# Performance work log

Measured on AMD Instinct MI355X. Metric: run time of the kernel, lower is better.

The kernel has to match this reference:

```python
import jax, jax.numpy as jnp
import numpy as np

B, S, D, H = 2, 2048, 2048, 16
HD = D // H  # head_dim = 128
ROPE_BASE = 10000.0


def _rope_tables(seq_len, head_dim, base, dtype):
    inv_freq = 1.0 / (base ** (jnp.arange(0, head_dim, 2, dtype=jnp.float32) / head_dim))
    t = jnp.arange(seq_len, dtype=jnp.float32)
    freqs = jnp.einsum('s,d->sd', t, inv_freq)           # [S, HD/2]
    emb = jnp.concatenate([freqs, freqs], axis=-1)        # [S, HD]
    return jnp.cos(emb).astype(dtype), jnp.sin(emb).astype(dtype)


def _rotate_half(x):
    half = x.shape[-1] // 2
    return jnp.concatenate([-x[..., half:], x[..., :half]], axis=-1)


def setup_inputs() -> dict:
    key = jax.random.key(0)
    kx, kq, kk, kv, ko = jax.random.split(key, 5)
    std = 0.02
    return {
        'x': jax.random.normal(kx, (B, S, D), dtype=jnp.float32),
        'Wq': jax.random.normal(kq, (D, D), dtype=jnp.float32) * std,
        'Wk': jax.random.normal(kk, (D, D), dtype=jnp.float32) * std,
        'Wv': jax.random.normal(kv, (D, D), dtype=jnp.float32) * std,
        'Wo': jax.random.normal(ko, (D, D), dtype=jnp.float32) * std,
    }


def reference(x, Wq, Wk, Wv, Wo):
    b, s, d = x.shape
    scale = HD ** -0.5
    # projections (nn.Linear: x @ W.T), split heads -> [b, h, s, hd]
    q = (x @ Wq.T).reshape(b, s, H, HD).transpose(0, 2, 1, 3)
    k = (x @ Wk.T).reshape(b, s, H, HD).transpose(0, 2, 1, 3)
    v = (x @ Wv.T).reshape(b, s, H, HD).transpose(0, 2, 1, 3)
    cos, sin = _rope_tables(s, HD, ROPE_BASE, x.dtype)    # [s, hd]
    q = q * cos + _rotate_half(q) * sin
    k = k * cos + _rotate_half(k) * sin
    scores = jnp.einsum('bhqd,bhkd->bhqk', q, k) * scale  # [b,h,s,s]
    causal = jnp.triu(jnp.ones((s, s), dtype=bool), k=1)
    scores = jnp.where(causal, jnp.float32(-jnp.inf).astype(scores.dtype), scores)
    attn = jax.nn.softmax(scores, axis=-1)
    out = jnp.einsum('bhqk,bhkd->bhqd', attn, v)
    out = out.transpose(0, 2, 1, 3).reshape(b, s, d)
    return out @ Wo.T
```

## Files before the change

### kernel.cpp

```cpp
#include <hip/hip_runtime.h>
#include <hip/hip_bf16.h>
#include <cstdint>
#include <cstddef>

#define B_ 2
#define S_ 2048
#define D_ 2048
#define H_ 16
#define HD_ 128

typedef __bf16 bf16_t;
typedef __bf16 bf16x8 __attribute__((ext_vector_type(8)));
typedef __bf16 bf16x4 __attribute__((ext_vector_type(4)));
typedef short s16x4 __attribute__((ext_vector_type(4)));
typedef float f32x4 __attribute__((ext_vector_type(4)));

__device__ __forceinline__ void async16(const bf16_t* g, bf16_t* l) {
    __builtin_amdgcn_global_load_lds(
        (const __attribute__((address_space(1))) unsigned int*)g,
        (__attribute__((address_space(3))) unsigned int*)l, 16, 0, 0);
}

__device__ __forceinline__ f32x4 mfma16x16x16_bf16(bf16x4 a, bf16x4 b, f32x4 c) {
#if __has_builtin(__builtin_amdgcn_mfma_f32_16x16x16_bf16)
    return __builtin_amdgcn_mfma_f32_16x16x16_bf16(a, b, c, 0, 0, 0);
#elif __has_builtin(__builtin_amdgcn_mfma_f32_16x16x16bf16_1k)
    return __builtin_amdgcn_mfma_f32_16x16x16bf16_1k(
        __builtin_bit_cast(s16x4, a), __builtin_bit_cast(s16x4, b), c, 0, 0, 0);
#else
    f32x4 d = c;
    asm("v_mfma_f32_16x16x16_bf16 %0, %1, %2, %0" : "+v"(d) : "v"(a), "v"(b));
    return d;
#endif
}

__global__ void f2b_multi(const float* __restrict__ x, const float* __restrict__ wq,
                          const float* __restrict__ wk, const float* __restrict__ wv,
                          const float* __restrict__ wo, bf16_t* __restrict__ xb,
                          bf16_t* __restrict__ wqb, bf16_t* __restrict__ wkb,
                          bf16_t* __restrict__ wvb, bf16_t* __restrict__ wob) {
    const float* in; bf16_t* out;
    float sc = 1.0f;
    switch (blockIdx.y) {
        case 0: in = x;            out = xb;            break;
        case 1: in = x + 4194304;  out = xb + 4194304;  break;
        case 2: in = wq;           out = wqb; sc = 0.08838834764831845f; break;
        case 3: in = wk;           out = wkb;           break;
        case 4: in = wv;           out = wvb;           break;
        default: in = wo;          out = wob;           break;
    }
    int i = (blockIdx.x * blockDim.x + threadIdx.x) * 4;
    float4 v = *(const float4*)(in + i);
    bf16x4 o = { (bf16_t)(v.x * sc), (bf16_t)(v.y * sc), (bf16_t)(v.z * sc), (bf16_t)(v.w * sc) };
    *(bf16x4*)(out + i) = o;
}

__global__ void rope_kernel(bf16_t* __restrict__ q, bf16_t* __restrict__ k) {
    int idx = blockIdx.x * blockDim.x + threadIdx.x;
    bf16_t* p = (blockIdx.y == 0) ? q : k;
    int i0 = (idx & 7) * 8;
    int rest = idx >> 3;
    int h = rest & (H_ - 1);
    int row = rest >> 4;
    int s = row & (S_ - 1);
    size_t base = (size_t)row * D_ + (size_t)h * HD_ + i0;
    bf16x8 x0 = *(bf16x8*)(p + base);
    bf16x8 x1 = *(bf16x8*)(p + base + 64);
    bf16x8 o0, o1;
#pragma unroll
    for (int j = 0; j < 8; ++j) {
        float inv = __expf(-(float)(i0 + j) * 0.14391156831212787f);
        float ang = (float)s * inv;
        float sn, c;
        __sincosf(ang, &sn, &c);
        float a = (float)x0[j], bb = (float)x1[j];
        o0[j] = (bf16_t)(a * c - bb * sn);
        o1[j] = (bf16_t)(bb * c + a * sn);
    }
    *(bf16x8*)(p + base) = o0;
    *(bf16x8*)(p + base + 64) = o1;
}


__global__ __launch_bounds__(256) void gemm_qkv(const bf16_t* __restrict__ A,
                                                const bf16_t* __restrict__ Wq,
                                                const bf16_t* __restrict__ Wk,
                                                const bf16_t* __restrict__ Wv,
                                                bf16_t* __restrict__ qb,
                                                bf16_t* __restrict__ kb,
                                                bf16_t* __restrict__ vtb) {
    __shared__ __align__(16) bf16_t As[128 * 64];
    __shared__ __align__(16) bf16_t Bs[128 * 64];
    const int K = D_;
    int t = threadIdx.x;
    int w = t >> 6, lane = t & 63, lo = lane & 15, hi = lane >> 4;
    int seg = blockIdx.x >> 4;
    int n0 = (blockIdx.x & 15) * 128;
    int m0 = blockIdx.y * 128;
    const bf16_t* Bt = (seg == 0) ? Wq : (seg == 1) ? Wk : Wv;
    int wm = (w & 1) * 64, wn = (w >> 1) * 64;
    f32x4 acc[4][4] = {};
    int srow = w * 32 + (lane >> 3);
    int scol = ((lane & 7) ^ (lane >> 3)) * 8;
    const bf16_t* gA = A  + (size_t)(m0 + srow) * K + scol;
    const bf16_t* gB = Bt + (size_t)(n0 + srow) * K + scol;
    bf16_t* lA = As + w * 2048 + lane * 8;
    bf16_t* lB = Bs + w * 2048 + lane * 8;
    for (int k0 = 0; k0 < K; k0 += 64) {
#pragma unroll
        for (int i = 0; i < 4; ++i) {
            async16(gA + (size_t)(i * 8) * K + k0, lA + i * 512);
            async16(gB + (size_t)(i * 8) * K + k0, lB + i * 512);
        }
        __syncthreads();
#pragma unroll
        for (int kk = 0; kk < 2; ++kk) {
            bf16x8 af[4], bfr[4];
            int pc = (kk * 4 + hi) ^ (lo & 7);
#pragma unroll
            for (int ms = 0; ms < 4; ++ms)
                af[ms] = *(const bf16x8*)(As + (wm + ms * 16 + lo) * 64 + pc * 8);
#pragma unroll
            for (int ns = 0; ns < 4; ++ns)
                bfr[ns] = *(const bf16x8*)(Bs + (wn + ns * 16 + lo) * 64 + pc * 8);
#pragma unroll
            for (int ms = 0; ms < 4; ++ms)
#pragma unroll
                for (int ns = 0; ns < 4; ++ns)
                    acc[ms][ns] = __builtin_amdgcn_mfma_f32_16x16x32_bf16(af[ms], bfr[ns], acc[ms][ns], 0, 0, 0);
        }
        __syncthreads();
    }
    if (seg < 2) {
        bf16_t* C = (seg == 0) ? qb : kb;
#pragma unroll
        for (int ms = 0; ms < 4; ++ms)
#pragma unroll
            for (int ns = 0; ns < 4; ++ns)
#pragma unroll
                for (int r = 0; r < 4; ++r)
                    C[(size_t)(m0 + wm + ms * 16 + hi * 4 + r) * D_ + n0 + wn + ns * 16 + lo] = (bf16_t)acc[ms][ns][r];
    } else {
#pragma unroll
        for (int ms = 0; ms < 4; ++ms) {
            int mrow = m0 + wm + ms * 16 + hi * 4;
            int bb = mrow >> 11, s = mrow & (S_ - 1);
#pragma unroll
            for (int ns = 0; ns < 4; ++ns) {
                int d = n0 + wn + ns * 16 + lo;
                bf16x4 pv = { (bf16_t)acc[ms][ns][0], (bf16_t)acc[ms][ns][1],
                              (bf16_t)acc[ms][ns][2], (bf16_t)acc[ms][ns][3] };
                *(bf16x4*)(vtb + (size_t)bb * D_ * S_ + (size_t)d * S_ + s) = pv;
            }
        }
    }
}

__global__ __launch_bounds__(256) void gemm_bt_f32(const bf16_t* __restrict__ A,
                                                   const bf16_t* __restrict__ Bt,
                                                   float* __restrict__ C,
                                                   int M, int N, int K) {
    __shared__ __align__(16) bf16_t As[128 * 64];
    __shared__ __align__(16) bf16_t Bs[128 * 64];
    int t = threadIdx.x;
    int w = t >> 6, lane = t & 63, lo = lane & 15, hi = lane >> 4;
    int m0 = blockIdx.y * 128, n0 = blockIdx.x * 128;
    int wm = (w & 1) * 64, wn = (w >> 1) * 64;
    f32x4 acc[4][4] = {};
    int srow = w * 32 + (lane >> 3);
    int scol = ((lane & 7) ^ (lane >> 3)) * 8;
    const bf16_t* gA = A  + (size_t)(m0 + srow) * K + scol;
    const bf16_t* gB = Bt + (size_t)(n0 + srow) * K + scol;
    bf16_t* lA = As + w * 2048 + lane * 8;
    bf16_t* lB = Bs + w * 2048 + lane * 8;
    for (int k0 = 0; k0 < K; k0 += 64) {
#pragma unroll
        for (int i = 0; i < 4; ++i) {
            async16(gA + (size_t)(i * 8) * K + k0, lA + i * 512);
            async16(gB + (size_t)(i * 8) * K + k0, lB + i * 512);
        }
        __syncthreads();
#pragma unroll
        for (int kk = 0; kk < 2; ++kk) {
            bf16x8 af[4], bfr[4];
            int pc = (kk * 4 + hi) ^ (lo & 7);
#pragma unroll
            for (int ms = 0; ms < 4; ++ms)
                af[ms] = *(const bf16x8*)(As + (wm + ms * 16 + lo) * 64 + pc * 8);
#pragma unroll
            for (int ns = 0; ns < 4; ++ns)
                bfr[ns] = *(const bf16x8*)(Bs + (wn + ns * 16 + lo) * 64 + pc * 8);
#pragma unroll
            for (int ms = 0; ms < 4; ++ms)
#pragma unroll
                for (int ns = 0; ns < 4; ++ns)
                    acc[ms][ns] = __builtin_amdgcn_mfma_f32_16x16x32_bf16(af[ms], bfr[ns], acc[ms][ns], 0, 0, 0);
        }
        __syncthreads();
    }
#pragma unroll
    for (int ms = 0; ms < 4; ++ms)
#pragma unroll
        for (int ns = 0; ns < 4; ++ns)
#pragma unroll
            for (int r = 0; r < 4; ++r)
                C[(size_t)(m0 + wm + ms * 16 + hi * 4 + r) * N + n0 + wn + ns * 16 + lo] = acc[ms][ns][r];
}

__global__ __launch_bounds__(512) void attn_kernel(const bf16_t* __restrict__ q,
                                                   const bf16_t* __restrict__ k,
                                                   const bf16_t* __restrict__ vt,
                                                   bf16_t* __restrict__ o) {
    __shared__ __align__(16) bf16_t Ks[2][128 * 128];
    __shared__ __align__(16) bf16_t Vs[2][128 * 128];
    int t = threadIdx.x;
    int w = t >> 6, lane = t & 63, lo = lane & 15, hi = lane >> 4;
    int bx = blockIdx.x;
    int b = blockIdx.y >> 4, h = blockIdx.y & 15;
    const size_t head_off = (size_t)b * S_ * D_ + (size_t)h * HD_;
    const size_t vhead_off = ((size_t)b * D_ + (size_t)h * HD_) * S_;

#pragma unroll 1
    for (int pass = 0; pass < 2; ++pass) {
        int qt = pass ? (15 - bx) : bx;
        int q0 = qt * 128;
        int qg = q0 + w * 16 + lo;
        bf16x8 aq[4];
#pragma unroll
        for (int c = 0; c < 4; ++c)
            aq[c] = *(const bf16x8*)(q + head_off + (size_t)qg * D_ + c * 32 + hi * 8);

        float l_part = 0.f;
        f32x4 oacc[8] = {};
        int nkt = qt + 1;

        {
#pragma unroll
            for (int i = 0; i < 4; ++i) {
                int chunk = w * 4 + i;
                int r = chunk * 4 + hi;
                async16(k + head_off + (size_t)r * D_ + (lo ^ (r & 15)) * 8,
                        Ks[0] + chunk * 512 + lane * 8);
            }
#pragma unroll
            for (int i = 0; i < 4; ++i) {
                int chunk = w * 4 + i;
                int d = chunk * 4 + hi;
                async16(vt + vhead_off + (size_t)d * S_ + (lo ^ (d & 15)) * 8,
                        Vs[0] + chunk * 512 + lane * 8);
            }
        }
        __syncthreads();

        for (int kt = 0; kt < nkt; ++kt) {
            int k0 = kt * 128;
            int cb = kt & 1;
            if (kt + 1 < nkt) {
                int kn = k0 + 128;
#pragma unroll
                for (int i = 0; i < 4; ++i) {
                    int chunk = w * 4 + i;
                    int r = chunk * 4 + hi;
                    async16(k + head_off + (size_t)(kn + r) * D_ + (lo ^ (r & 15)) * 8,
                            Ks[cb ^ 1] + chunk * 512 + lane * 8);
                }
#pragma unroll
                for (int i = 0; i < 4; ++i) {
                    int chunk = w * 4 + i;
                    int d = chunk * 4 + hi;
                    async16(vt + vhead_off + (size_t)d * S_ + kn + (lo ^ (d & 15)) * 8,
                            Vs[cb ^ 1] + chunk * 512 + lane * 8);
                }
            }

            const bf16_t* Kb = Ks[cb];
            const bf16_t* Vb = Vs[cb];
            f32x4 sacc[8] = {};
#pragma unroll
            for (int c = 0; c < 4; ++c) {
#pragma unroll
                for (int nt = 0; nt < 8; ++nt) {
                    int row = nt * 16 + lo;
                    int pc = (c * 4 + hi) ^ lo;
                    bf16x8 ak = *(const bf16x8*)(Kb + row * 128 + pc * 8);
                    sacc[nt] = __builtin_amdgcn_mfma_f32_16x16x32_bf16(ak, aq[c], sacc[nt], 0, 0, 0);
                }
            }
            bool diag = (kt == qt);
            bf16x4 pf[8];
#pragma unroll
            for (int nt = 0; nt < 8; ++nt) {
#pragma unroll
                for (int r = 0; r < 4; ++r) {
                    float e = __expf(fminf(sacc[nt][r], 60.f));
                    if (diag) {
                        int kg = k0 + nt * 16 + hi * 4 + r;
                        if (kg > qg) e = 0.f;
                    }
                    l_part += e;
                    pf[nt][r] = (bf16_t)e;
                }
            }
#pragma unroll
            for (int nt = 0; nt < 8; ++nt) {
                int kkb = nt * 16 + hi * 4;
                int c16 = kkb >> 3, rem = kkb & 7;
#pragma unroll
                for (int dt = 0; dt < 8; ++dt) {
                    int d = dt * 16 + lo;
                    bf16x4 av = *(const bf16x4*)(Vb + d * 128 + (c16 ^ (d & 15)) * 8 + rem);
                    oacc[dt] = mfma16x16x16_bf16(av, pf[nt], oacc[dt]);
                }
            }
            __syncthreads();
        }
        float l = l_part;
        l += __shfl_xor(l, 16);
        l += __shfl_xor(l, 32);
        float rl = 1.0f / l;
#pragma unroll
        for (int dt = 0; dt < 8; ++dt) {
            bf16x4 ov = { (bf16_t)(oacc[dt][0] * rl), (bf16_t)(oacc[dt][1] * rl),
                          (bf16_t)(oacc[dt][2] * rl), (bf16_t)(oacc[dt][3] * rl) };
            *(bf16x4*)(o + head_off + (size_t)qg * D_ + dt * 16 + hi * 4) = ov;
        }
    }
}

extern "C" void kernel_launch(void* const* d_in, const int* in_sizes, int n_in,
                              void* d_out, int out_size, void* d_ws, size_t ws_size,
                              hipStream_t stream) {
    (void)in_sizes; (void)n_in; (void)out_size; (void)ws_size;
    const float* x  = (const float*)d_in[0];
    const float* Wq = (const float*)d_in[1];
    const float* Wk = (const float*)d_in[2];
    const float* Wv = (const float*)d_in[3];
    const float* Wo = (const float*)d_in[4];
    char* ws = (char*)d_ws;
    bf16_t* xb  = (bf16_t*)(ws);
    bf16_t* Wqb = (bf16_t*)(ws + 16777216);
    bf16_t* Wkb = (bf16_t*)(ws + 25165824);
    bf16_t* Wvb = (bf16_t*)(ws + 33554432);
    bf16_t* Wob = (bf16_t*)(ws + 41943040);
    bf16_t* qb  = (bf16_t*)(ws + 50331648);
    bf16_t* kb  = (bf16_t*)(ws + 67108864);
    bf16_t* vtb = (bf16_t*)(ws + 83886080);
    bf16_t* ob  = (bf16_t*)(ws + 100663296);
    float* out = (float*)d_out;

    f2b_multi<<<dim3(4096, 6), 256, 0, stream>>>(x, Wq, Wk, Wv, Wo, xb, Wqb, Wkb, Wvb, Wob);

    gemm_qkv<<<dim3(48, 32), 256, 0, stream>>>(xb, Wqb, Wkb, Wvb, qb, kb, vtb);

    rope_kernel<<<dim3((B_ * S_ * H_ * 8) / 256, 2), 256, 0, stream>>>(qb, kb);

    attn_kernel<<<dim3(8, B_ * H_), 512, 0, stream>>>(qb, kb, vtb, ob);

    gemm_bt_f32<<<dim3(D_ / 128, (B_ * S_) / 128), 256, 0, stream>>>(ob, Wob, out, B_ * S_, D_, D_);
}
```

Baseline: 371.4 us.

## Pipeline QKV GEMM with triple-buffered async LDS loads and larger 128x256 tiles

```diff
diff --git a/kernel.cpp b/kernel.cpp
--- a/kernel.cpp
+++ b/kernel.cpp
@@ -81,56 +81,121 @@
     *(bf16x8*)(p + base + 64) = o1;
 }
 
-
-__global__ __launch_bounds__(256) void gemm_qkv(const bf16_t* __restrict__ A,
-                                                const bf16_t* __restrict__ Wq,
-                                                const bf16_t* __restrict__ Wk,
-                                                const bf16_t* __restrict__ Wv,
-                                                bf16_t* __restrict__ qb,
-                                                bf16_t* __restrict__ kb,
-                                                bf16_t* __restrict__ vtb) {
-    __shared__ __align__(16) bf16_t As[128 * 64];
-    __shared__ __align__(16) bf16_t Bs[128 * 64];
+__global__ __launch_bounds__(512, 2) void gemm_qkv(const bf16_t* __restrict__ A,
+                                                   const bf16_t* __restrict__ Wq,
+                                                   const bf16_t* __restrict__ Wk,
+                                                   const bf16_t* __restrict__ Wv,
+                                                   bf16_t* __restrict__ qb,
+                                                   bf16_t* __restrict__ kb,
+                                                   bf16_t* __restrict__ vtb) {
+    __shared__ __align__(16) bf16_t lds[3 * 24576];
     const int K = D_;
+    const int NT = K / 64;
     int t = threadIdx.x;
     int w = t >> 6, lane = t & 63, lo = lane & 15, hi = lane >> 4;
-    int seg = blockIdx.x >> 4;
-    int n0 = (blockIdx.x & 15) * 128;
+    int seg = blockIdx.x >> 3;
+    int n0 = (blockIdx.x & 7) * 256;
     int m0 = blockIdx.y * 128;
     const bf16_t* Bt = (seg == 0) ? Wq : (seg == 1) ? Wk : Wv;
-    int wm = (w & 1) * 64, wn = (w >> 1) * 64;
+    int wm = w >> 2, wn = w & 3;
     f32x4 acc[4][4] = {};
-    int srow = w * 32 + (lane >> 3);
-    int scol = ((lane & 7) ^ (lane >> 3)) * 8;
+    int srow = t >> 3;
+    int scol = ((t & 7) ^ ((t >> 3) & 7)) * 8;
     const bf16_t* gA = A  + (size_t)(m0 + srow) * K + scol;
     const bf16_t* gB = Bt + (size_t)(n0 + srow) * K + scol;
-    bf16_t* lA = As + w * 2048 + lane * 8;
-    bf16_t* lB = Bs + w * 2048 + lane * 8;
-    for (int k0 = 0; k0 < K; k0 += 64) {
-#pragma unroll
-        for (int i = 0; i < 4; ++i) {
-            async16(gA + (size_t)(i * 8) * K + k0, lA + i * 512);
-            async16(gB + (size_t)(i * 8) * K + k0, lB + i * 512);
-        }
-        __syncthreads();
-#pragma unroll
-        for (int kk = 0; kk < 2; ++kk) {
-            bf16x8 af[4], bfr[4];
-            int pc = (kk * 4 + hi) ^ (lo & 7);
-#pragma unroll
-            for (int ms = 0; ms < 4; ++ms)
-                af[ms] = *(const bf16x8*)(As + (wm + ms * 16 + lo) * 64 + pc * 8);
+    const int dA = t * 8;
+    const int dB = 8192 + t * 8;
+
+#pragma unroll
+    for (int tt0 = 0; tt0 < 2; ++tt0) {
+        bf16_t* base = lds + tt0 * 24576;
+        int k0 = tt0 * 64;
+        async16(gA + k0, base + dA);
+        async16(gA + (size_t)64 * K + k0, base + dA + 4096);
+#pragma unroll
+        for (int s = 0; s < 4; ++s)
+            async16(gB + (size_t)(s * 64) * K + k0, base + dB + s * 4096);
+    }
+    asm volatile("s_waitcnt vmcnt(6)" ::: "memory");
+    __builtin_amdgcn_sched_barrier(0);
+    __builtin_amdgcn_s_barrier();
+
+    int cur = 0;
+#pragma unroll 1
+    for (int tt = 0; tt < NT; ++tt) {
+        const bf16_t* Ab = lds + cur * 24576;
+        const bf16_t* Bb = Ab + 8192;
+        int nb = cur + 2; if (nb >= 3) nb -= 3;
+        bf16_t* sb = lds + nb * 24576;
+        int k2 = (tt + 2) * 64;
+        bool st = (tt + 2 < NT);
+
+        {
+            bf16x8 af[4], bfv[4];
+            int pc = hi ^ (lo & 7);
+#pragma unroll
+            for (int ms = 0; ms < 4; ++ms)
+                af[ms] = *(const bf16x8*)(Ab + (wm * 64 + ms * 16 + lo) * 64 + pc * 8);
 #pragma unroll
             for (int ns = 0; ns < 4; ++ns)
-                bfr[ns] = *(const bf16x8*)(Bs + (wn + ns * 16 + lo) * 64 + pc * 8);
+                bfv[ns] = *(const bf16x8*)(Bb + (wn * 64 + ns * 16 + lo) * 64 + pc * 8);
+            if (st) {
+                async16(gA + k2, sb + dA);
+                async16(gA + (size_t)64 * K + k2, sb + dA + 4096);
+                async16(gB + k2, sb + dB);
+            }
+            __builtin_amdgcn_sched_barrier(0);
+            __builtin_amdgcn_s_barrier();
+            asm volatile("s_waitcnt lgkmcnt(0)" ::: "memory");
+            __builtin_amdgcn_sched_barrier(0);
+            __builtin_amdgcn_s_setprio(1);
 #pragma unroll
             for (int ms = 0; ms < 4; ++ms)
 #pragma unroll
                 for (int ns = 0; ns < 4; ++ns)
-                    acc[ms][ns] = __builtin_amdgcn_mfma_f32_16x16x32_bf16(af[ms], bfr[ns], acc[ms][ns], 0, 0, 0);
-        }
-        __syncthreads();
-    }
+                    acc[ms][ns] = __builtin_amdgcn_mfma_f32_16x16x32_bf16(
+                        af[ms], bfv[ns], acc[ms][ns], 0, 0, 0);
+            __builtin_amdgcn_s_setprio(0);
+            __builtin_amdgcn_sched_barrier(0);
+            __builtin_amdgcn_s_barrier();
+        }
+        {
+            bf16x8 af[4], bfv[4];
+            int pc = (4 + hi) ^ (lo & 7);
+#pragma unroll
+            for (int ms = 0; ms < 4; ++ms)
+                af[ms] = *(const bf16x8*)(Ab + (wm * 64 + ms * 16 + lo) * 64 + pc * 8);
+#pragma unroll
+            for (int ns = 0; ns < 4; ++ns)
+                bfv[ns] = *(const bf16x8*)(Bb + (wn * 64 + ns * 16 + lo) * 64 + pc * 8);
+            if (st) {
+                async16(gB + (size_t)64 * K + k2, sb + dB + 4096);
+                async16(gB + (size_t)128 * K + k2, sb + dB + 8192);
+                async16(gB + (size_t)192 * K + k2, sb + dB + 12288);
+            }
+            __builtin_amdgcn_sched_barrier(0);
+            __builtin_amdgcn_s_barrier();
+            asm volatile("s_waitcnt lgkmcnt(0)" ::: "memory");
+            __builtin_amdgcn_sched_barrier(0);
+            __builtin_amdgcn_s_setprio(1);
+#pragma unroll
+            for (int ms = 0; ms < 4; ++ms)
+#pragma unroll
+                for (int ns = 0; ns < 4; ++ns)
+                    acc[ms][ns] = __builtin_amdgcn_mfma_f32_16x16x32_bf16(
+                        af[ms], bfv[ns], acc[ms][ns], 0, 0, 0);
+            __builtin_amdgcn_s_setprio(0);
+            __builtin_amdgcn_sched_barrier(0);
+            if (st)
+                asm volatile("s_waitcnt vmcnt(6)" ::: "memory");
+            else if (tt + 1 < NT)
+                asm volatile("s_waitcnt vmcnt(0)" ::: "memory");
+            __builtin_amdgcn_sched_barrier(0);
+            __builtin_amdgcn_s_barrier();
+        }
+        cur = cur + 1; if (cur == 3) cur = 0;
+    }
+
     if (seg < 2) {
         bf16_t* C = (seg == 0) ? qb : kb;
 #pragma unroll
@@ -139,15 +204,16 @@
             for (int ns = 0; ns < 4; ++ns)
 #pragma unroll
                 for (int r = 0; r < 4; ++r)
-                    C[(size_t)(m0 + wm + ms * 16 + hi * 4 + r) * D_ + n0 + wn + ns * 16 + lo] = (bf16_t)acc[ms][ns][r];
+                    C[(size_t)(m0 + wm * 64 + ms * 16 + hi * 4 + r) * D_ + n0 + wn * 64 + ns * 16 + lo] =
+                        (bf16_t)acc[ms][ns][r];
     } else {
 #pragma unroll
         for (int ms = 0; ms < 4; ++ms) {
-            int mrow = m0 + wm + ms * 16 + hi * 4;
+            int mrow = m0 + wm * 64 + ms * 16 + hi * 4;
             int bb = mrow >> 11, s = mrow & (S_ - 1);
 #pragma unroll
             for (int ns = 0; ns < 4; ++ns) {
-                int d = n0 + wn + ns * 16 + lo;
+                int d = n0 + wn * 64 + ns * 16 + lo;
                 bf16x4 pv = { (bf16_t)acc[ms][ns][0], (bf16_t)acc[ms][ns][1],
                               (bf16_t)acc[ms][ns][2], (bf16_t)acc[ms][ns][3] };
                 *(bf16x4*)(vtb + (size_t)bb * D_ * S_ + (size_t)d * S_ + s) = pv;
@@ -350,7 +416,7 @@
 
     f2b_multi<<<dim3(4096, 6), 256, 0, stream>>>(x, Wq, Wk, Wv, Wo, xb, Wqb, Wkb, Wvb, Wob);
 
-    gemm_qkv<<<dim3(48, 32), 256, 0, stream>>>(xb, Wqb, Wkb, Wvb, qb, kb, vtb);
+    gemm_qkv<<<dim3(24, 32), 512, 0, stream>>>(xb, Wqb, Wkb, Wvb, qb, kb, vtb);
 
     rope_kernel<<<dim3((B_ * S_ * H_ * 8) / 256, 2), 256, 0, stream>>>(qb, kb);
 
```

Result: no change. 374.8 us (+0.9%).

## Fuse RoPE into QKV GEMM epilogue via LDS half-exchange

Applied to the files above, without the earlier changes.

```diff
diff --git a/kernel.cpp b/kernel.cpp
--- a/kernel.cpp
+++ b/kernel.cpp
@@ -55,32 +55,6 @@
     *(bf16x4*)(out + i) = o;
 }
 
-__global__ void rope_kernel(bf16_t* __restrict__ q, bf16_t* __restrict__ k) {
-    int idx = blockIdx.x * blockDim.x + threadIdx.x;
-    bf16_t* p = (blockIdx.y == 0) ? q : k;
-    int i0 = (idx & 7) * 8;
-    int rest = idx >> 3;
-    int h = rest & (H_ - 1);
-    int row = rest >> 4;
-    int s = row & (S_ - 1);
-    size_t base = (size_t)row * D_ + (size_t)h * HD_ + i0;
-    bf16x8 x0 = *(bf16x8*)(p + base);
-    bf16x8 x1 = *(bf16x8*)(p + base + 64);
-    bf16x8 o0, o1;
-#pragma unroll
-    for (int j = 0; j < 8; ++j) {
-        float inv = __expf(-(float)(i0 + j) * 0.14391156831212787f);
-        float ang = (float)s * inv;
-        float sn, c;
-        __sincosf(ang, &sn, &c);
-        float a = (float)x0[j], bb = (float)x1[j];
-        o0[j] = (bf16_t)(a * c - bb * sn);
-        o1[j] = (bf16_t)(bb * c + a * sn);
-    }
-    *(bf16x8*)(p + base) = o0;
-    *(bf16x8*)(p + base + 64) = o1;
-}
-
 
 __global__ __launch_bounds__(256) void gemm_qkv(const bf16_t* __restrict__ A,
                                                 const bf16_t* __restrict__ Wq,
@@ -89,8 +63,9 @@
                                                 bf16_t* __restrict__ qb,
                                                 bf16_t* __restrict__ kb,
                                                 bf16_t* __restrict__ vtb) {
-    __shared__ __align__(16) bf16_t As[128 * 64];
-    __shared__ __align__(16) bf16_t Bs[128 * 64];
+    __shared__ __align__(16) bf16_t sbuf[2 * 128 * 64];
+    bf16_t* As = sbuf;
+    bf16_t* Bs = sbuf + 8192;
     const int K = D_;
     int t = threadIdx.x;
     int w = t >> 6, lane = t & 63, lo = lane & 15, hi = lane >> 4;
@@ -131,16 +106,8 @@
         }
         __syncthreads();
     }
-    if (seg < 2) {
-        bf16_t* C = (seg == 0) ? qb : kb;
-#pragma unroll
-        for (int ms = 0; ms < 4; ++ms)
-#pragma unroll
-            for (int ns = 0; ns < 4; ++ns)
-#pragma unroll
-                for (int r = 0; r < 4; ++r)
-                    C[(size_t)(m0 + wm + ms * 16 + hi * 4 + r) * D_ + n0 + wn + ns * 16 + lo] = (bf16_t)acc[ms][ns][r];
-    } else {
+
+    if (seg == 2) {
 #pragma unroll
         for (int ms = 0; ms < 4; ++ms) {
             int mrow = m0 + wm + ms * 16 + hi * 4;
@@ -151,6 +118,74 @@
                 bf16x4 pv = { (bf16_t)acc[ms][ns][0], (bf16_t)acc[ms][ns][1],
                               (bf16_t)acc[ms][ns][2], (bf16_t)acc[ms][ns][3] };
                 *(bf16x4*)(vtb + (size_t)bb * D_ * S_ + (size_t)d * S_ + s) = pv;
+            }
+        }
+        return;
+    }
+
+    bf16_t* C = (seg == 0) ? qb : kb;
+    f32x4* xt = (f32x4*)sbuf;
+    int slot = w & 1;
+    bool upper = (wn != 0);
+
+    if (upper) {
+#pragma unroll
+        for (int ms = 0; ms < 4; ++ms)
+#pragma unroll
+            for (int ns = 0; ns < 4; ++ns) {
+                int c = ns * 16 + lo, j = ms * 4 + hi;
+                xt[slot * 1024 + c * 16 + (j ^ (c & 15))] = acc[ms][ns];
+            }
+    }
+    __syncthreads();
+    if (!upper) {
+#pragma unroll
+        for (int ns = 0; ns < 4; ++ns) {
+            int c = ns * 16 + lo;
+            float inv = __expf(-(float)c * 0.14391156831212787f);
+#pragma unroll
+            for (int ms = 0; ms < 4; ++ms) {
+                int j = ms * 4 + hi;
+                f32x4 pv = xt[slot * 1024 + c * 16 + (j ^ (c & 15))];
+#pragma unroll
+                for (int r = 0; r < 4; ++r) {
+                    int row = m0 + wm + ms * 16 + hi * 4 + r;
+                    float ang = (float)(row & (S_ - 1)) * inv;
+                    float sn, cs;
+                    __sincosf(ang, &sn, &cs);
+                    C[(size_t)row * D_ + n0 + c] = (bf16_t)(acc[ms][ns][r] * cs - pv[r] * sn);
+                }
+            }
+        }
+    }
+    __syncthreads();
+    if (!upper) {
+#pragma unroll
+        for (int ms = 0; ms < 4; ++ms)
+#pragma unroll
+            for (int ns = 0; ns < 4; ++ns) {
+                int c = ns * 16 + lo, j = ms * 4 + hi;
+                xt[slot * 1024 + c * 16 + (j ^ (c & 15))] = acc[ms][ns];
+            }
+    }
+    __syncthreads();
+    if (upper) {
+#pragma unroll
+        for (int ns = 0; ns < 4; ++ns) {
+            int c = ns * 16 + lo;
+            float inv = __expf(-(float)c * 0.14391156831212787f);
+#pragma unroll
+            for (int ms = 0; ms < 4; ++ms) {
+                int j = ms * 4 + hi;
+                f32x4 pv = xt[slot * 1024 + c * 16 + (j ^ (c & 15))];
+#pragma unroll
+                for (int r = 0; r < 4; ++r) {
+                    int row = m0 + wm + ms * 16 + hi * 4 + r;
+                    float ang = (float)(row & (S_ - 1)) * inv;
+                    float sn, cs;
+                    __sincosf(ang, &sn, &cs);
+                    C[(size_t)row * D_ + n0 + 64 + c] = (bf16_t)(acc[ms][ns][r] * cs + pv[r] * sn);
+                }
             }
         }
     }
@@ -352,8 +387,6 @@
 
     gemm_qkv<<<dim3(48, 32), 256, 0, stream>>>(xb, Wqb, Wkb, Wvb, qb, kb, vtb);
 
-    rope_kernel<<<dim3((B_ * S_ * H_ * 8) / 256, 2), 256, 0, stream>>>(qb, kb);
-
     attn_kernel<<<dim3(8, B_ * H_), 512, 0, stream>>>(qb, kb, vtb, ob);
 
     gemm_bt_f32<<<dim3(D_ / 128, (B_ * S_) / 128), 256, 0, stream>>>(ob, Wob, out, B_ * S_, D_, D_);
```

Result: no change. 371.8 us (+0.1%).
